# Performance work log

Hardware: AMD Instinct MI355X
Metric: run time of the kernel (lower is better)

## Reference

```python
import jax, jax.numpy as jnp
import numpy as np

B, N, D = 128, 196, 1024          # batch, num image features, d_model == hidden_dim
E = 1024                           # embed_dim
V = 10000                          # vocab_size
NH = 8                             # num_heads
T = 20                             # max caption length
DH = D // NH


def setup_inputs() -> dict:
    key = jax.random.key(0)
    ks = jax.random.split(key, 16)
    u = lambda k, shape, s=0.1: jax.random.uniform(k, shape, jnp.float32, -s, s)
    lengths = jnp.sort(jax.random.randint(ks[1], (B,), 1, T + 1))[::-1]
    lengths = lengths.at[0].set(T)  # ensure max(lengths) == T
    return {
        "enc_features": jax.random.normal(ks[0], (B, N, D), jnp.float32),
        "captions": jax.random.randint(ks[2], (B, T), 0, V),
        "lengths": lengths,
        "embed_W": u(ks[3], (V, E)),
        # LSTMCell params (PyTorch layout: gates ordered i,f,g,o)
        "W_ih": u(ks[4], (4 * D, E + D), 0.03),
        "b_ih": u(ks[5], (4 * D,), 0.03),
        "W_hh": u(ks[6], (4 * D, D), 0.03),
        "b_hh": u(ks[7], (4 * D,), 0.03),
        # AoA block
        "Wq": u(ks[8], (D, D), 0.03), "bq": jnp.zeros((D,), jnp.float32),
        "Wk": u(ks[9], (D, D), 0.03), "bk": jnp.zeros((D,), jnp.float32),
        "Wv": u(ks[10], (D, D), 0.03), "bv": jnp.zeros((D,), jnp.float32),
        "W_aoa": u(ks[11], (2 * D, 2 * D), 0.02), "b_aoa": jnp.zeros((2 * D,), jnp.float32),
        # weight-normed predict layer (dim=0): W = g * v / ||v||_row
        "pred_v": u(ks[12], (V, D)),
        "pred_g": jnp.ones((V,), jnp.float32),
        "pred_b": jnp.zeros((V,), jnp.float32),
    }


def reference(enc_features, captions, lengths, embed_W, W_ih, b_ih, W_hh, b_hh,
              Wq, bq, Wk, bk, Wv, bv, W_aoa, b_aoa, pred_v, pred_g, pred_b):
    # eval mode: dropouts are identity; ss_prob == 0.
    scale = 1.0 / jnp.sqrt(jnp.asarray(DH, jnp.float32))
    mean_f = jnp.mean(enc_features, axis=1)                      # [B, D]
    # K/V projections of enc_features are step-invariant: hoist out of the loop.
    K = (enc_features @ Wk.T + bk).reshape(B, N, NH, DH).transpose(0, 2, 1, 3)  # [B,NH,N,DH]
    Vv = (enc_features @ Wv.T + bv).reshape(B, N, NH, DH).transpose(0, 2, 1, 3)
    # weight-norm predict matrix (dim=0 row-wise norm)
    Wn = pred_g[:, None] * pred_v / jnp.linalg.norm(pred_v, axis=1, keepdims=True)  # [V, D]

    active = (jnp.arange(T)[:, None] < lengths[None, :])         # [T, B]
    toks = captions.T                                            # [T, B]

    def step(carry, inp):
        h, m, ctx = carry
        it, act = inp
        emb = embed_W[it]                                        # [B, E]
        x = jnp.concatenate([emb, mean_f + ctx], axis=-1)        # [B, E+D]
        gates = x @ W_ih.T + b_ih + h @ W_hh.T + b_hh            # [B, 4D]
        i, f, g, o = jnp.split(gates, 4, axis=-1)
        m2 = jax.nn.sigmoid(f) * m + jax.nn.sigmoid(i) * jnp.tanh(g)
        h2 = jax.nn.sigmoid(o) * jnp.tanh(m2)                    # [B, D]
        # single-query multi-head attention
        q = (h2 @ Wq.T + bq).reshape(B, NH, DH)                  # [B, NH, DH]
        scores = jnp.einsum('bhd,bhnd->bhn', q, K) * scale       # [B, NH, N]
        p = jax.nn.softmax(scores, axis=-1)
        att = jnp.einsum('bhn,bhnd->bhd', p, Vv).reshape(B, D)   # [B, D]
        # AoA: Linear(2D->2D) + GLU on cat(att, query)
        a = jnp.concatenate([att, h2], axis=-1) @ W_aoa.T + b_aoa
        a1, a2 = jnp.split(a, 2, axis=-1)
        ctx2 = a1 * jax.nn.sigmoid(a2)                           # [B, D]
        preds = ctx2 @ Wn.T + pred_b                             # [B, V]
        preds = jnp.where(act[:, None], preds, 0.0)
        return (h2, m2, ctx2), preds

    z = jnp.zeros((B, D), jnp.float32)
    _, preds = jax.lax.scan(step, (z, z, z), (toks, active))     # [T, B, V]
    return preds.transpose(1, 0, 2)                              # [B, T, V], zero-padded
```

## Files before the change

kernel.cpp:

```cpp
#include <hip/hip_runtime.h>
#include <hip/hip_bf16.h>
#include <cstdint>

#define BB 128
#define TT 20
#define VV 10000
#define DD 1024
#define NHH 8
#define DHH 128
#define NN 196

typedef float f32x4 __attribute__((ext_vector_type(4)));
typedef __bf16 bf16x8 __attribute__((ext_vector_type(8)));
typedef unsigned int u32x4 __attribute__((ext_vector_type(4)));
typedef unsigned int u32x2 __attribute__((ext_vector_type(2)));

__device__ __forceinline__ unsigned short f2bf(float x) {
  unsigned u = __float_as_uint(x);
  u += 0x7FFFu + ((u >> 16) & 1u);
  return (unsigned short)(u >> 16);
}
__device__ __forceinline__ float bf2f(unsigned short h) {
  return __uint_as_float(((unsigned)h) << 16);
}
__device__ __forceinline__ float sigm(float x) { return 1.f / (1.f + __expf(-x)); }
__device__ __forceinline__ unsigned pk2(float lo, float hi) {
  return (unsigned)f2bf(lo) | ((unsigned)f2bf(hi) << 16);
}
__device__ __forceinline__ int xcd_swz(int orig, int nb) {
  int q = nb >> 3, r = nb & 7;
  int x = orig & 7, i = orig >> 3;
  return (x < r ? x * (q + 1) : r * (q + 1) + (x - r) * q) + i;
}
__device__ __forceinline__ void gl16(const void* g, void* l) {
  __builtin_amdgcn_global_load_lds((const __attribute__((address_space(1))) void*)g,
                                   (__attribute__((address_space(3))) void*)l, 16, 0, 0);
}

template<int N> __device__ __forceinline__ void waitvm() {
  if constexpr (N == 0)       asm volatile("s_waitcnt vmcnt(0)" ::: "memory");
  else if constexpr (N == 3)  asm volatile("s_waitcnt vmcnt(3)" ::: "memory");
  else if constexpr (N == 5)  asm volatile("s_waitcnt vmcnt(5)" ::: "memory");
  else if constexpr (N == 6)  asm volatile("s_waitcnt vmcnt(6)" ::: "memory");
  else if constexpr (N == 8)  asm volatile("s_waitcnt vmcnt(8)" ::: "memory");
  else if constexpr (N == 10) asm volatile("s_waitcnt vmcnt(10)" ::: "memory");
  else if constexpr (N == 12) asm volatile("s_waitcnt vmcnt(12)" ::: "memory");
  else if constexpr (N == 16) asm volatile("s_waitcnt vmcnt(16)" ::: "memory");
}
#define LGKM0()  asm volatile("s_waitcnt lgkmcnt(0)" ::: "memory")
#define SCHED0() __builtin_amdgcn_sched_barrier(0)

template<int BM, int BN, int MODE, int DEP, bool RF, bool K2 = false>
__launch_bounds__(256)
__global__ void gemmp(const unsigned short* __restrict__ A, int lda,
                      const unsigned short* __restrict__ W, int ldw,
                      int nkt, int N, int ncol,
                      const float* __restrict__ bias,
                      float* __restrict__ outF, unsigned short* __restrict__ outB,
                      float* __restrict__ mbuf, const float* __restrict__ meanf,
                      unsigned short* __restrict__ xaoa, unsigned short* __restrict__ xn2,
                      const int* __restrict__ lengths)
{
  constexpr int SZA = BM * 128;
  constexpr int SZB = BN * 128;
  constexpr int NJ = BN / 16;
  constexpr int MI = BM / 64;
  constexpr int S = BM / 32 + BN / 32;
  __shared__ char smem[DEP * (SZA + SZB)];

  const int nb = gridDim.x;
  const int wg = xcd_swz(blockIdx.x, nb);
  int xi, rowt;
  if (RF) { const int nrow = nb / ncol; rowt = wg % nrow; xi = wg / nrow; }
  else    { xi = wg % ncol; rowt = wg / ncol; }
  const int colbase = xi * BN;
  const int rowbase = rowt * BM;
  const int tid = threadIdx.x;
  const int lane = tid & 63, wv = tid >> 6;
  const int wrow = wv * (BM / 4);
  const int lr = lane & 15;
  const int srow = lane >> 3;
  const int schunk = ((lane & 7) ^ srow) * 8;

  auto stage = [&](int t, int buf) {
    char* sA = smem + buf * (SZA + SZB);
    char* sB = sA + SZA;
    const int k0 = t << 6;
    #pragma unroll
    for (int s = 0; s < BM / 32; ++s) {
      const int rb = s * 32 + wv * 8;
      gl16(A + (size_t)(rowbase + rb + srow) * lda + k0 + schunk, sA + rb * 128);
    }
    #pragma unroll
    for (int s = 0; s < BN / 32; ++s) {
      const int rb = s * 32 + wv * 8;
      int br = colbase + rb + srow;
      if (MODE == 2) br = br < N ? br : N - 1;
      gl16(W + (size_t)br * ldw + k0 + schunk, sB + rb * 128);
    }
  };

  f32x4 acc[MI][NJ];
  const f32x4 zero = {0.f, 0.f, 0.f, 0.f};
  #pragma unroll
  for (int i = 0; i < MI; ++i)
    #pragma unroll
    for (int j = 0; j < NJ; ++j) acc[i][j] = zero;

  #pragma unroll
  for (int t = 0; t < (K2 ? 4 : DEP); ++t) stage(t, t);

  const int axor = (lr & 7) << 4;
  const int ccol = (lane >> 4) * 16;

  if constexpr (K2) {
    for (int i = 0; i < nkt; i += 2) {
      if (i + 2 < nkt) waitvm<2 * S>(); else waitvm<0>();
      __builtin_amdgcn_s_barrier();
      SCHED0();
      if (i + 4 < nkt) {
        stage(i + 4, (i + 4) % DEP);
        stage(i + 5, (i + 5) % DEP);
      }
      bf16x8 af[2][MI][2], bfr[2][NJ][2];
      #pragma unroll
      for (int u = 0; u < 2; ++u) {
        const char* sA = smem + ((i + u) % DEP) * (SZA + SZB);
        const char* sB = sA + SZA;
        #pragma unroll
        for (int ii = 0; ii < MI; ++ii)
          #pragma unroll
          for (int kk = 0; kk < 2; ++kk)
            af[u][ii][kk] = *reinterpret_cast<const bf16x8*>(
                sA + (wrow + ii * 16 + lr) * 128 + ((kk * 64 + ccol) ^ axor));
        #pragma unroll
        for (int j = 0; j < NJ; ++j)
          #pragma unroll
          for (int kk = 0; kk < 2; ++kk)
            bfr[u][j][kk] = *reinterpret_cast<const bf16x8*>(
                sB + (j * 16 + lr) * 128 + ((kk * 64 + ccol) ^ axor));
      }
      LGKM0();
      SCHED0();
      #pragma unroll
      for (int u = 0; u < 2; ++u)
        #pragma unroll
        for (int kk = 0; kk < 2; ++kk)
          #pragma unroll
          for (int ii = 0; ii < MI; ++ii)
            #pragma unroll
            for (int j = 0; j < NJ; ++j)
              acc[ii][j] = __builtin_amdgcn_mfma_f32_16x16x32_bf16(af[u][ii][kk], bfr[u][j][kk], acc[ii][j], 0, 0, 0);
    }
  } else {
    int buf = 0;
    for (int i = 0; i < nkt; ++i) {
      const int rem = nkt - 1 - i;
      if (rem >= DEP - 1)            waitvm<S * (DEP - 1)>();
      else if (DEP > 2 && rem == 1)  waitvm<S>();
      else                           waitvm<0>();
      __builtin_amdgcn_s_barrier();
      SCHED0();
      const char* sA = smem + buf * (SZA + SZB);
      const char* sB = sA + SZA;
      bf16x8 af[MI][2], bfr[NJ][2];
      #pragma unroll
      for (int ii = 0; ii < MI; ++ii)
        #pragma unroll
        for (int kk = 0; kk < 2; ++kk)
          af[ii][kk] = *reinterpret_cast<const bf16x8*>(
              sA + (wrow + ii * 16 + lr) * 128 + ((kk * 64 + ccol) ^ axor));
      #pragma unroll
      for (int j = 0; j < NJ; ++j)
        #pragma unroll
        for (int kk = 0; kk < 2; ++kk)
          bfr[j][kk] = *reinterpret_cast<const bf16x8*>(
              sB + (j * 16 + lr) * 128 + ((kk * 64 + ccol) ^ axor));
      LGKM0();
      SCHED0();
      __builtin_amdgcn_s_barrier();
      SCHED0();
      if (i + DEP < nkt) stage(i + DEP, buf);
      #pragma unroll
      for (int kk = 0; kk < 2; ++kk)
        #pragma unroll
        for (int ii = 0; ii < MI; ++ii)
          #pragma unroll
          for (int j = 0; j < NJ; ++j)
            acc[ii][j] = __builtin_amdgcn_mfma_f32_16x16x32_bf16(af[ii][kk], bfr[j][kk], acc[ii][j], 0, 0, 0);
      buf = (buf == DEP - 1) ? 0 : buf + 1;
    }
  }

  const int rg4 = (lane >> 4) * 4;

  if constexpr (MODE == 0) {
    #pragma unroll
    for (int ii = 0; ii < MI; ++ii)
      #pragma unroll
      for (int j = 0; j < NJ; ++j) {
        const int gcol = colbase + j * 16 + lr;
        #pragma unroll
        for (int r = 0; r < 4; ++r)
          outF[(size_t)(rowbase + wrow + ii * 16 + rg4 + r) * N + gcol] = acc[ii][j][r];
      }
  } else if constexpr (MODE == 1) {
    #pragma unroll
    for (int ii = 0; ii < MI; ++ii)
      #pragma unroll
      for (int j = 0; j < NJ; ++j) {
        const int gcol = colbase + j * 16 + lr;
        const float bv = bias[gcol];
        #pragma unroll
        for (int r = 0; r < 4; ++r)
          outB[(size_t)(rowbase + wrow + ii * 16 + rg4 + r) * N + gcol] = f2bf(acc[ii][j][r] + bv);
      }
  } else if constexpr (MODE == 2) {
    #pragma unroll
    for (int ii = 0; ii < MI; ++ii)
      #pragma unroll
      for (int j = 0; j < NJ; ++j) {
        const int gcol = colbase + j * 16 + lr;
        if (gcol >= N) continue;
        const float bv = bias[gcol];
        #pragma unroll
        for (int r = 0; r < 4; ++r) {
          const int gr = rowbase + wrow + ii * 16 + rg4 + r;
          const int tt = gr >> 7, bb = gr & 127;
          outF[((size_t)bb * TT + tt) * VV + gcol] =
              (tt < lengths[bb]) ? acc[ii][j][r] + bv : 0.f;
        }
      }
  } else if constexpr (MODE == 3) {
    const float b0 = bias[colbase + lr], b1 = bias[colbase + 16 + lr];
    float a0[MI][4], a1[MI][4];
    #pragma unroll
    for (int ii = 0; ii < MI; ++ii)
      #pragma unroll
      for (int r = 0; r < 4; ++r) {
        const int grow = rowbase + wrow + ii * 16 + rg4 + r;
        a0[ii][r] = acc[ii][0][r] + b0 + outF[(size_t)grow * 4096 + colbase + lr];
        a1[ii][r] = acc[ii][1][r] + b1 + outF[(size_t)grow * 4096 + colbase + 16 + lr];
      }
    const int d = (colbase >> 2) + (lr & 7);
    #pragma unroll
    for (int ii = 0; ii < MI; ++ii)
      #pragma unroll
      for (int r = 0; r < 4; ++r) {
        const float fg = __shfl_xor(a0[ii][r], 8);
        const float og = __shfl_xor(a1[ii][r], 8);
        if (lr < 8) {
          const int grow = rowbase + wrow + ii * 16 + rg4 + r;
          const float m2 = sigm(fg) * mbuf[(size_t)grow * DD + d] + sigm(a0[ii][r]) * tanhf(a1[ii][r]);
          const float h2 = sigm(og) * tanhf(m2);
          mbuf[(size_t)grow * DD + d] = m2;
          const unsigned short hb = f2bf(h2);
          xaoa[(size_t)grow * 2048 + 1024 + d] = hb;
          xn2[(size_t)grow * 2048 + 1024 + d] = hb;
        }
      }
  } else {
    const int d = (colbase >> 1) + lr;
    const float b0 = bias[colbase + lr], b1 = bias[colbase + 16 + lr];
    #pragma unroll
    for (int ii = 0; ii < MI; ++ii)
      #pragma unroll
      for (int r = 0; r < 4; ++r) {
        const int grow = rowbase + wrow + ii * 16 + rg4 + r;
        const float av1 = acc[ii][0][r] + b0;
        const float av2 = acc[ii][1][r] + b1;
        const float c2 = av1 * sigm(av2);
        outB[(size_t)grow * DD + d] = f2bf(c2);
        xn2[(size_t)grow * 2048 + d] = f2bf(meanf[(size_t)grow * DD + d] + c2);
      }
  }
}

__launch_bounds__(256)
__global__ void attn_kernel(const float* __restrict__ qbuf, const float* __restrict__ bq,
                            const unsigned short* __restrict__ KV, unsigned short* __restrict__ xaoa) {
  const int bh = blockIdx.x, b = bh >> 3, h = bh & 7;
  const int tid = threadIdx.x;
  const int lane = tid & 63, wv = tid >> 6;
  __shared__ float qs[DHH];
  __shared__ float sc[NN + 4];
  __shared__ float pvred[2][DHH];
  __shared__ float redm[4], reds[4];
  if (tid < DHH)
    qs[tid] = bq[h * DHH + tid] + qbuf[(size_t)b * DD + h * DHH + tid];
  __syncthreads();
  if (tid < NN) {
    const unsigned short* kr = KV + ((size_t)(b * NN + tid)) * 2048 + h * DHH;
    float a = 0.f;
    #pragma unroll
    for (int j = 0; j < 16; ++j) {
      u32x4 kk = *reinterpret_cast<const u32x4*>(kr + j * 8);
      #pragma unroll
      for (int w = 0; w < 4; ++w) {
        a += bf2f((unsigned short)(kk[w] & 0xffffu)) * qs[j * 8 + w * 2]
           + bf2f((unsigned short)(kk[w] >> 16)) * qs[j * 8 + w * 2 + 1];
      }
    }
    sc[tid] = a * 0.08838834764831845f;
  }
  __syncthreads();
  float v = (tid < NN) ? sc[tid] : -1e30f;
  #pragma unroll
  for (int o = 32; o; o >>= 1) v = fmaxf(v, __shfl_xor(v, o));
  if (lane == 0) redm[wv] = v;
  __syncthreads();
  const float mx = fmaxf(fmaxf(redm[0], redm[1]), fmaxf(redm[2], redm[3]));
  float e = 0.f;
  if (tid < NN) { e = __expf(sc[tid] - mx); sc[tid] = e; }
  float s = e;
  #pragma unroll
  for (int o = 32; o; o >>= 1) s += __shfl_xor(s, o);
  if (lane == 0) reds[wv] = s;
  __syncthreads();
  const float inv = 1.f / (reds[0] + reds[1] + reds[2] + reds[3]);
  const int d = tid & 127, half = tid >> 7;
  const unsigned short* vr = KV + ((size_t)(b * NN + half * 98)) * 2048 + 1024 + h * DHH + d;
  const float* pr = sc + half * 98;
  float a0 = 0.f, a1 = 0.f;
  #pragma unroll 7
  for (int n = 0; n < 98; n += 2) {
    a0 += pr[n]     * bf2f(vr[(size_t)n * 2048]);
    a1 += pr[n + 1] * bf2f(vr[(size_t)(n + 1) * 2048]);
  }
  pvred[half][d] = a0 + a1;
  __syncthreads();
  if (tid < DHH)
    xaoa[(size_t)b * 2048 + h * DHH + tid] = f2bf((pvred[0][tid] + pvred[1][tid]) * inv);
}

__launch_bounds__(256)
__global__ void prep_kernel(const float* __restrict__ W_ih, const float* __restrict__ W_hh,
                            const float* __restrict__ Wq, const float* __restrict__ W_aoa,
                            const float* __restrict__ Wk, const float* __restrict__ Wv,
                            const float* __restrict__ b_ih, const float* __restrict__ b_hh,
                            const float* __restrict__ b_aoa, const float* __restrict__ bk,
                            const float* __restrict__ bv,
                            const float* __restrict__ embed_W, const int* __restrict__ captions,
                            const float* __restrict__ meanf,
                            unsigned short* __restrict__ WcatI, unsigned short* __restrict__ Wq_b,
                            unsigned short* __restrict__ WaoaI, unsigned short* __restrict__ Wkv_b,
                            float* __restrict__ bcombI, float* __restrict__ baoaI,
                            float* __restrict__ bkv,
                            unsigned short* __restrict__ embAll, float* __restrict__ mbuf,
                            unsigned short* __restrict__ x2_0)
{
  const int bid = blockIdx.x, tid = threadIdx.x;
  if (bid < 12288) {
    int i = bid * 256 + tid;
    int rp = i / 768, c4 = (i - rp * 768) * 4;
    int rem = rp & 31, g = rem >> 3, d = (rp >> 5) * 8 + (rem & 7);
    int orig = g * 1024 + d;
    const float* src = (c4 < 2048) ? (W_ih + (size_t)orig * 2048 + c4)
                                   : (W_hh + (size_t)orig * 1024 + (c4 - 2048));
    f32x4 vv = *reinterpret_cast<const f32x4*>(src);
    u32x2 o = { pk2(vv[0], vv[1]), pk2(vv[2], vv[3]) };
    *reinterpret_cast<u32x2*>(WcatI + (size_t)rp * 3072 + c4) = o;
  } else if (bid < 13312) {
    int i = (bid - 12288) * 256 + tid;
    f32x4 vv = *reinterpret_cast<const f32x4*>(Wq + (size_t)i * 4);
    u32x2 o = { pk2(vv[0], vv[1]), pk2(vv[2], vv[3]) };
    *reinterpret_cast<u32x2*>(Wq_b + (size_t)i * 4) = o;
  } else if (bid < 17408) {
    int i = (bid - 13312) * 256 + tid;
    int rp = i >> 9, c4 = (i & 511) * 4;
    int rem = rp & 31, half = rem >> 4, d = (rp >> 5) * 16 + (rem & 15);
    int orig = half * 1024 + d;
    f32x4 vv = *reinterpret_cast<const f32x4*>(W_aoa + (size_t)orig * 2048 + c4);
    u32x2 o = { pk2(vv[0], vv[1]), pk2(vv[2], vv[3]) };
    *reinterpret_cast<u32x2*>(WaoaI + (size_t)rp * 2048 + c4) = o;
  } else if (bid < 19456) {
    int i = (bid - 17408) * 256 + tid;
    int row = i >> 8, c4 = (i & 255) << 2;
    const float* src = (row < 1024) ? (Wk + (size_t)row * 1024 + c4)
                                    : (Wv + (size_t)(row - 1024) * 1024 + c4);
    f32x4 vv = *reinterpret_cast<const f32x4*>(src);
    u32x2 o = { pk2(vv[0], vv[1]), pk2(vv[2], vv[3]) };
    *reinterpret_cast<u32x2*>(Wkv_b + (size_t)row * 1024 + c4) = o;
  } else if (bid < 19472) {
    int i = (bid - 19456) * 256 + tid;
    {
      int rem = i & 31, g = rem >> 3, d = (i >> 5) * 8 + (rem & 7);
      int orig = g * 1024 + d;
      bcombI[i] = b_ih[orig] + b_hh[orig];
    }
    if (i < 2048) {
      int rem = i & 31, half = rem >> 4, d = (i >> 5) * 16 + (rem & 15);
      baoaI[i] = b_aoa[half * 1024 + d];
      bkv[i] = (i < 1024) ? bk[i] : bv[i - 1024];
    }
  } else if (bid < 22032) {
    int i = (bid - 19472) * 256 + tid;
    int j4 = (i & 255) << 2, b = (i >> 8) & 127, t = i >> 15;
    int tok = captions[b * TT + t];
    f32x4 vv = *reinterpret_cast<const f32x4*>(embed_W + (size_t)tok * DD + j4);
    u32x2 o = { pk2(vv[0], vv[1]), pk2(vv[2], vv[3]) };
    *reinterpret_cast<u32x2*>(embAll + ((size_t)t * BB + b) * DD + j4) = o;
  } else {
    int idx = (bid - 22032) * 256 + tid;
    int b = idx >> 10, d = idx & 1023;
    mbuf[idx] = 0.f;
    x2_0[(size_t)b * 2048 + d] = f2bf(meanf[idx]);
    x2_0[(size_t)b * 2048 + 1024 + d] = 0;
  }
}

__launch_bounds__(256)
__global__ void meanconv_kernel(const float* __restrict__ enc, float* __restrict__ meanf,
                                unsigned short* __restrict__ encb) {
  int b = blockIdx.x >> 2, d = (blockIdx.x & 3) * 256 + threadIdx.x;
  const float* p = enc + (size_t)b * NN * DD + d;
  unsigned short* q = encb + (size_t)b * NN * DD + d;
  float s = 0.f;
  for (int n = 0; n < NN; ++n) {
    float x = p[(size_t)n * DD];
    s += x;
    q[(size_t)n * DD] = f2bf(x);
  }
  meanf[(size_t)b * DD + d] = s * (1.0f / (float)NN);
}

__launch_bounds__(256)
__global__ void wn_kernel(const float* __restrict__ pred_v, const float* __restrict__ pred_g,
                          unsigned short* __restrict__ Wn) {
  int v = blockIdx.x, tid = threadIdx.x;
  f32x4 x = *reinterpret_cast<const f32x4*>(pred_v + (size_t)v * DD + tid * 4);
  float s = x[0] * x[0] + x[1] * x[1] + x[2] * x[2] + x[3] * x[3];
  #pragma unroll
  for (int o = 32; o; o >>= 1) s += __shfl_down(s, o);
  __shared__ float red[4];
  if ((tid & 63) == 0) red[tid >> 6] = s;
  __syncthreads();
  float inv = pred_g[v] * rsqrtf(red[0] + red[1] + red[2] + red[3]);
  u32x2 o = { pk2(x[0] * inv, x[1] * inv), pk2(x[2] * inv, x[3] * inv) };
  *reinterpret_cast<u32x2*>(Wn + (size_t)v * DD + tid * 4) = o;
}

extern "C" void kernel_launch(void* const* d_in, const int* in_sizes, int n_in,
                              void* d_out, int out_size, void* d_ws, size_t ws_size,
                              hipStream_t stream) {
  const float* enc      = (const float*)d_in[0];
  const int*   captions = (const int*)d_in[1];
  const int*   lengths  = (const int*)d_in[2];
  const float* embed_W  = (const float*)d_in[3];
  const float* W_ih     = (const float*)d_in[4];
  const float* b_ih     = (const float*)d_in[5];
  const float* W_hh     = (const float*)d_in[6];
  const float* b_hh     = (const float*)d_in[7];
  const float* Wq       = (const float*)d_in[8];
  const float* bq       = (const float*)d_in[9];
  const float* Wk       = (const float*)d_in[10];
  const float* bk       = (const float*)d_in[11];
  const float* Wv       = (const float*)d_in[12];
  const float* bv       = (const float*)d_in[13];
  const float* W_aoa    = (const float*)d_in[14];
  const float* b_aoa    = (const float*)d_in[15];
  const float* pred_v   = (const float*)d_in[16];
  const float* pred_g   = (const float*)d_in[17];
  const float* pred_b   = (const float*)d_in[18];
  float* out = (float*)d_out;

  char* base = (char*)d_ws;
  size_t off = 0;
  auto alloc = [&](size_t bytes) -> char* {
    char* p = base + off;
    off = (off + bytes + 255) & ~(size_t)255;
    return p;
  };
  unsigned short* KV     = (unsigned short*)alloc((size_t)BB * NN * 2048 * 2);
  unsigned short* WcatI  = (unsigned short*)alloc((size_t)4096 * 3072 * 2);
  unsigned short* WaoaI  = (unsigned short*)alloc((size_t)2048 * 2048 * 2);
  unsigned short* Wq_b   = (unsigned short*)alloc((size_t)DD * DD * 2);
  unsigned short* Wkv_b  = (unsigned short*)alloc((size_t)2048 * 1024 * 2);
  float* bcombI          = (float*)alloc(4096 * 4);
  float* baoaI           = (float*)alloc(2048 * 4);
  float* bkv             = (float*)alloc(2048 * 4);
  float* meanf           = (float*)alloc((size_t)BB * DD * 4);
  float* mbuf            = (float*)alloc((size_t)BB * DD * 4);
  unsigned short* embAll = (unsigned short*)alloc((size_t)TT * BB * DD * 2);
  unsigned short* x2     = (unsigned short*)alloc((size_t)2 * BB * 2048 * 2);
  char* uni = alloc((size_t)BB * NN * DD * 2);
  unsigned short* encb = (unsigned short*)uni;
  size_t ua = 0;
  auto carve = [&](size_t b) -> char* { char* p = uni + ua; ua = (ua + b + 255) & ~(size_t)255; return p; };
  float* Eall               = (float*)carve((size_t)TT * BB * 4096 * 4);
  unsigned short* predinAll = (unsigned short*)carve((size_t)TT * BB * DD * 2);
  unsigned short* xaoa      = (unsigned short*)carve((size_t)BB * 2048 * 2);
  float* qbuf               = (float*)carve((size_t)BB * DD * 4);
  unsigned short* Wn_b      = (unsigned short*)uni;
  if (off > ws_size || ua > (size_t)BB * NN * DD * 2) return;

  meanconv_kernel<<<512, 256, 0, stream>>>(enc, meanf, encb);
  prep_kernel<<<22544, 256, 0, stream>>>(W_ih, W_hh, Wq, W_aoa, Wk, Wv,
                                         b_ih, b_hh, b_aoa, bk, bv,
                                         embed_W, captions, meanf,
                                         WcatI, Wq_b, WaoaI, Wkv_b,
                                         bcombI, baoaI, bkv, embAll, mbuf, x2);
  gemmp<128, 128, 1, 2, false><<<3136, 256, 0, stream>>>(encb, 1024, Wkv_b, 1024, 16, 2048, 16, bkv,
                                                         nullptr, KV, nullptr, nullptr, nullptr, nullptr, nullptr);
  gemmp<128, 128, 0, 2, true><<<640, 256, 0, stream>>>(embAll, 1024, WcatI, 3072, 16, 4096, 32, nullptr,
                                                       Eall, nullptr, nullptr, nullptr, nullptr, nullptr, nullptr);

  for (int t = 0; t < TT; ++t) {
    unsigned short* xc = x2 + (size_t)(t & 1) * BB * 2048;
    unsigned short* xn = x2 + (size_t)((t + 1) & 1) * BB * 2048;
    gemmp<64, 32, 3, 6, false, true><<<256, 256, 0, stream>>>(xc, 2048, WcatI + 1024, 3072, 32, 4096, 128, bcombI,
                                                              Eall + (size_t)t * BB * 4096, nullptr, mbuf, nullptr, xaoa, xn, nullptr);
    gemmp<64, 32, 0, 6, false, true><<<64, 256, 0, stream>>>(xaoa + 1024, 2048, Wq_b, 1024, 16, 1024, 32, nullptr,
                                                             qbuf, nullptr, nullptr, nullptr, nullptr, nullptr, nullptr);
    attn_kernel<<<BB * NHH, 256, 0, stream>>>(qbuf, bq, KV, xaoa);
    gemmp<64, 32, 4, 6, false, true><<<128, 256, 0, stream>>>(xaoa, 2048, WaoaI, 2048, 32, 2048, 64, baoaI,
                                                              nullptr, predinAll + (size_t)t * BB * DD, nullptr, meanf, nullptr, xn, nullptr);
  }

  wn_kernel<<<VV, 256, 0, stream>>>(pred_v, pred_g, Wn_b);
  gemmp<128, 128, 2, 2, true><<<1580, 256, 0, stream>>>(predinAll, 1024, Wn_b, 1024, 16, VV, 79, pred_b,
                                                        out, nullptr, nullptr, nullptr, nullptr, nullptr, lengths);
}
```

Baseline: 1.169 ms.

## Fuse mean/convert into prep kernel and merge KV and embedding GEMMs into one launch

```diff
diff --git a/kernel.cpp b/kernel.cpp
--- a/kernel.cpp
+++ b/kernel.cpp
@@ -204,17 +204,6 @@
         for (int r = 0; r < 4; ++r)
           outF[(size_t)(rowbase + wrow + ii * 16 + rg4 + r) * N + gcol] = acc[ii][j][r];
       }
-  } else if constexpr (MODE == 1) {
-    #pragma unroll
-    for (int ii = 0; ii < MI; ++ii)
-      #pragma unroll
-      for (int j = 0; j < NJ; ++j) {
-        const int gcol = colbase + j * 16 + lr;
-        const float bv = bias[gcol];
-        #pragma unroll
-        for (int r = 0; r < 4; ++r)
-          outB[(size_t)(rowbase + wrow + ii * 16 + rg4 + r) * N + gcol] = f2bf(acc[ii][j][r] + bv);
-      }
   } else if constexpr (MODE == 2) {
     #pragma unroll
     for (int ii = 0; ii < MI; ++ii)
@@ -272,6 +261,128 @@
         const float c2 = av1 * sigm(av2);
         outB[(size_t)grow * DD + d] = f2bf(c2);
         xn2[(size_t)grow * 2048 + d] = f2bf(meanf[(size_t)grow * DD + d] + c2);
+      }
+  }
+}
+
+__device__ __forceinline__ void gemm_core128(const unsigned short* __restrict__ A, int lda,
+                                             const unsigned short* __restrict__ W, int ldw,
+                                             int rowbase, int colbase, char* smem,
+                                             f32x4 (&acc)[2][8])
+{
+  constexpr int SZA = 128 * 128, SZB = 128 * 128;
+  const int tid = threadIdx.x;
+  const int lane = tid & 63, wv = tid >> 6;
+  const int wrow = wv * 32;
+  const int lr = lane & 15;
+  const int srow = lane >> 3;
+  const int schunk = ((lane & 7) ^ srow) * 8;
+
+  auto stage = [&](int t, int buf) {
+    char* sA = smem + buf * (SZA + SZB);
+    char* sB = sA + SZA;
+    const int k0 = t << 6;
+    #pragma unroll
+    for (int s = 0; s < 4; ++s) {
+      const int rb = s * 32 + wv * 8;
+      gl16(A + (size_t)(rowbase + rb + srow) * lda + k0 + schunk, sA + rb * 128);
+    }
+    #pragma unroll
+    for (int s = 0; s < 4; ++s) {
+      const int rb = s * 32 + wv * 8;
+      gl16(W + (size_t)(colbase + rb + srow) * ldw + k0 + schunk, sB + rb * 128);
+    }
+  };
+
+  const f32x4 zero = {0.f, 0.f, 0.f, 0.f};
+  #pragma unroll
+  for (int i = 0; i < 2; ++i)
+    #pragma unroll
+    for (int j = 0; j < 8; ++j) acc[i][j] = zero;
+
+  stage(0, 0); stage(1, 1);
+  const int axor = (lr & 7) << 4;
+  const int ccol = (lane >> 4) * 16;
+  int buf = 0;
+  for (int i = 0; i < 16; ++i) {
+    if (i < 15) waitvm<8>(); else waitvm<0>();
+    __builtin_amdgcn_s_barrier();
+    SCHED0();
+    const char* sA = smem + buf * (SZA + SZB);
+    const char* sB = sA + SZA;
+    bf16x8 af[2][2], bfr[8][2];
+    #pragma unroll
+    for (int ii = 0; ii < 2; ++ii)
+      #pragma unroll
+      for (int kk = 0; kk < 2; ++kk)
+        af[ii][kk] = *reinterpret_cast<const bf16x8*>(
+            sA + (wrow + ii * 16 + lr) * 128 + ((kk * 64 + ccol) ^ axor));
+    #pragma unroll
+    for (int j = 0; j < 8; ++j)
+      #pragma unroll
+      for (int kk = 0; kk < 2; ++kk)
+        bfr[j][kk] = *reinterpret_cast<const bf16x8*>(
+            sB + (j * 16 + lr) * 128 + ((kk * 64 + ccol) ^ axor));
+    LGKM0();
+    SCHED0();
+    __builtin_amdgcn_s_barrier();
+    SCHED0();
+    if (i + 2 < 16) stage(i + 2, buf);
+    #pragma unroll
+    for (int kk = 0; kk < 2; ++kk)
+      #pragma unroll
+      for (int ii = 0; ii < 2; ++ii)
+        #pragma unroll
+        for (int j = 0; j < 8; ++j)
+          acc[ii][j] = __builtin_amdgcn_mfma_f32_16x16x32_bf16(af[ii][kk], bfr[j][kk], acc[ii][j], 0, 0, 0);
+    buf ^= 1;
+  }
+}
+
+__launch_bounds__(256)
+__global__ void kv_eall_kernel(const unsigned short* __restrict__ encb,
+                               const unsigned short* __restrict__ Wkv,
+                               const float* __restrict__ bkv,
+                               unsigned short* __restrict__ KV,
+                               const unsigned short* __restrict__ embAll,
+                               const unsigned short* __restrict__ WcatI,
+                               float* __restrict__ Eall)
+{
+  __shared__ char smem[2 * (128 * 128 + 128 * 128)];
+  f32x4 acc[2][8];
+  const int tid = threadIdx.x;
+  const int lane = tid & 63, wv = tid >> 6;
+  const int wrow = wv * 32, lr = lane & 15;
+  const int rg4 = (lane >> 4) * 4;
+
+  if (blockIdx.x < 3136) {
+    const int wg = xcd_swz(blockIdx.x, 3136);
+    const int xi = wg % 16, rowt = wg / 16;
+    const int colbase = xi * 128, rowbase = rowt * 128;
+    gemm_core128(encb, 1024, Wkv, 1024, rowbase, colbase, smem, acc);
+    #pragma unroll
+    for (int ii = 0; ii < 2; ++ii)
+      #pragma unroll
+      for (int j = 0; j < 8; ++j) {
+        const int gcol = colbase + j * 16 + lr;
+        const float bv = bkv[gcol];
+        #pragma unroll
+        for (int r = 0; r < 4; ++r)
+          KV[(size_t)(rowbase + wrow + ii * 16 + rg4 + r) * 2048 + gcol] = f2bf(acc[ii][j][r] + bv);
+      }
+  } else {
+    const int wg = xcd_swz(blockIdx.x - 3136, 640);
+    const int rowt = wg % 20, xi = wg / 20;
+    const int colbase = xi * 128, rowbase = rowt * 128;
+    gemm_core128(embAll, 1024, WcatI, 3072, rowbase, colbase, smem, acc);
+    #pragma unroll
+    for (int ii = 0; ii < 2; ++ii)
+      #pragma unroll
+      for (int j = 0; j < 8; ++j) {
+        const int gcol = colbase + j * 16 + lr;
+        #pragma unroll
+        for (int r = 0; r < 4; ++r)
+          Eall[(size_t)(rowbase + wrow + ii * 16 + rg4 + r) * 4096 + gcol] = acc[ii][j][r];
       }
   }
 }
@@ -341,13 +452,14 @@
                             const float* __restrict__ b_aoa, const float* __restrict__ bk,
                             const float* __restrict__ bv,
                             const float* __restrict__ embed_W, const int* __restrict__ captions,
-                            const float* __restrict__ meanf,
+                            const float* __restrict__ enc,
                             unsigned short* __restrict__ WcatI, unsigned short* __restrict__ Wq_b,
                             unsigned short* __restrict__ WaoaI, unsigned short* __restrict__ Wkv_b,
                             float* __restrict__ bcombI, float* __restrict__ baoaI,
                             float* __restrict__ bkv,
-                            unsigned short* __restrict__ embAll, float* __restrict__ mbuf,
-                            unsigned short* __restrict__ x2_0)
+                            unsigned short* __restrict__ embAll,
+                            float* __restrict__ meanf, unsigned short* __restrict__ encb,
+                            float* __restrict__ mbuf, unsigned short* __restrict__ x2_0)
 {
   const int bid = blockIdx.x, tid = threadIdx.x;
   if (bid < 12288) {
@@ -401,27 +513,22 @@
     u32x2 o = { pk2(vv[0], vv[1]), pk2(vv[2], vv[3]) };
     *reinterpret_cast<u32x2*>(embAll + ((size_t)t * BB + b) * DD + j4) = o;
   } else {
-    int idx = (bid - 22032) * 256 + tid;
-    int b = idx >> 10, d = idx & 1023;
-    mbuf[idx] = 0.f;
-    x2_0[(size_t)b * 2048 + d] = f2bf(meanf[idx]);
+    int rb = bid - 22032;
+    int b = rb >> 2, d = (rb & 3) * 256 + tid;
+    const float* p = enc + (size_t)b * NN * DD + d;
+    unsigned short* q = encb + (size_t)b * NN * DD + d;
+    float s = 0.f;
+    for (int n = 0; n < NN; ++n) {
+      float x = p[(size_t)n * DD];
+      s += x;
+      q[(size_t)n * DD] = f2bf(x);
+    }
+    const float mval = s * (1.0f / (float)NN);
+    meanf[(size_t)b * DD + d] = mval;
+    mbuf[(size_t)b * DD + d] = 0.f;
+    x2_0[(size_t)b * 2048 + d] = f2bf(mval);
     x2_0[(size_t)b * 2048 + 1024 + d] = 0;
   }
-}
-
-__launch_bounds__(256)
-__global__ void meanconv_kernel(const float* __restrict__ enc, float* __restrict__ meanf,
-                                unsigned short* __restrict__ encb) {
-  int b = blockIdx.x >> 2, d = (blockIdx.x & 3) * 256 + threadIdx.x;
-  const float* p = enc + (size_t)b * NN * DD + d;
-  unsigned short* q = encb + (size_t)b * NN * DD + d;
-  float s = 0.f;
-  for (int n = 0; n < NN; ++n) {
-    float x = p[(size_t)n * DD];
-    s += x;
-    q[(size_t)n * DD] = f2bf(x);
-  }
-  meanf[(size_t)b * DD + d] = s * (1.0f / (float)NN);
 }
 
 __launch_bounds__(256)
@@ -494,16 +601,24 @@
   unsigned short* Wn_b      = (unsigned short*)uni;
   if (off > ws_size || ua > (size_t)BB * NN * DD * 2) return;
 
-  meanconv_kernel<<<512, 256, 0, stream>>>(enc, meanf, encb);
+  {
+    ua = 0;
+    encb = (unsigned short*)carve((size_t)BB * NN * DD * 2);
+    Eall = (float*)alloc((size_t)TT * BB * 4096 * 4);
+    predinAll = (unsigned short*)alloc((size_t)TT * BB * DD * 2);
+    xaoa      = (unsigned short*)alloc((size_t)BB * 2048 * 2);
+    qbuf      = (float*)alloc((size_t)BB * DD * 4);
+    Wn_b      = (unsigned short*)uni;
+    if (off > ws_size) return;
+  }
+
   prep_kernel<<<22544, 256, 0, stream>>>(W_ih, W_hh, Wq, W_aoa, Wk, Wv,
                                          b_ih, b_hh, b_aoa, bk, bv,
-                                         embed_W, captions, meanf,
+                                         embed_W, captions, enc,
                                          WcatI, Wq_b, WaoaI, Wkv_b,
-                                         bcombI, baoaI, bkv, embAll, mbuf, x2);
-  gemmp<128, 128, 1, 2, false><<<3136, 256, 0, stream>>>(encb, 1024, Wkv_b, 1024, 16, 2048, 16, bkv,
-                                                         nullptr, KV, nullptr, nullptr, nullptr, nullptr, nullptr);
-  gemmp<128, 128, 0, 2, true><<<640, 256, 0, stream>>>(embAll, 1024, WcatI, 3072, 16, 4096, 32, nullptr,
-                                                       Eall, nullptr, nullptr, nullptr, nullptr, nullptr, nullptr);
+                                         bcombI, baoaI, bkv, embAll,
+                                         meanf, encb, mbuf, x2);
+  kv_eall_kernel<<<3776, 256, 0, stream>>>(encb, Wkv_b, bkv, KV, embAll, WcatI, Eall);
 
   for (int t = 0; t < TT; ++t) {
     unsigned short* xc = x2 + (size_t)(t & 1) * BB * 2048;
```

Result: no change. 1.169 ms (+0.1%).
